# Performance work log

Measured on AMD Instinct MI355X. Metric: run time of the kernel, lower is better.

Reference implementation:

```python
import jax, jax.numpy as jnp
import numpy as np

N_NODES = 100000
N_EDGES = 1600000
IN_DIM = 128
OUT_DIM = 64
SLOPE = 0.2


def setup_inputs() -> dict:
    key = jax.random.key(0)
    k1, k2, k3, k4 = jax.random.split(key, 4)
    h = jax.random.normal(k1, (N_NODES, IN_DIM), dtype=jnp.float32)
    W = jax.random.normal(k2, (OUT_DIM, IN_DIM), dtype=jnp.float32) * (1.0 / np.sqrt(IN_DIM))
    src = jax.random.randint(k3, (N_EDGES,), 0, N_NODES, dtype=jnp.int64)
    dst = jax.random.randint(k4, (N_EDGES,), 0, N_NODES, dtype=jnp.int64)
    return {"h": h, "W": W, "src": src, "dst": dst}


def reference(h, W, src, dst):
    n = h.shape[0]
    z = h @ W.T                                   # [N, out_dim]
    z_src = z[src]                                # [E, out_dim]
    z_dst = z[dst]                                # [E, out_dim]
    e = jax.nn.leaky_relu(jnp.sum(z_src * z_dst, axis=1), negative_slope=SLOPE)  # [E]
    # segment softmax over incoming edges of each destination node
    m = jax.ops.segment_max(e, dst, num_segments=n)        # [N], -inf for isolated nodes
    ex = jnp.exp(e - m[dst])                                # [E]
    denom = jax.ops.segment_sum(ex, dst, num_segments=n)    # [N]
    alpha = ex / denom[dst]                                 # [E]
    agg = jax.ops.segment_sum(alpha[:, None] * z_src, dst, num_segments=n)  # [N, out_dim]
    return jax.nn.elu(agg)
```

## Files before the change

### kernel.cpp

```cpp
#include <hip/hip_runtime.h>
#include <hip/hip_fp16.h>
#include <math.h>

#define SLOPE 0.2f
#define LOG2E 1.4426950408889634f

typedef _Float16 half8_t __attribute__((ext_vector_type(8)));
typedef float    f32x4_t __attribute__((ext_vector_type(4)));

__device__ __forceinline__ unsigned short pk_f16(float x) {
    return __half_as_ushort(__float2half(x));
}
__device__ __forceinline__ float f16f(unsigned int bits_lo16) {
    return __half2float(__ushort_as_half((unsigned short)(bits_lo16 & 0xFFFFu)));
}

__global__ __launch_bounds__(256) void wcvt_kernel(const float* __restrict__ W,
                                                   unsigned short* __restrict__ Wh,
                                                   int total4) {
    int i = blockIdx.x * 256 + threadIdx.x;
    if (i < total4) {
        float4 w = *(const float4*)(W + (size_t)i * 4);
        ushort4 o;
        o.x = pk_f16(w.x); o.y = pk_f16(w.y);
        o.z = pk_f16(w.z); o.w = pk_f16(w.w);
        *(ushort4*)(Wh + (size_t)i * 4) = o;
    }
}

__global__ __launch_bounds__(256, 8) void gemm_hist_kernel(const float* __restrict__ h,
                                                           const unsigned short* __restrict__ Wh,
                                                           unsigned short* __restrict__ zh,
                                                           const int* __restrict__ dst,
                                                           int* __restrict__ cnt8,
                                                           unsigned short* __restrict__ rank,
                                                           int n, int ne, int nGemm) {
    int r5 = blockIdx.x % 5;
    int g5 = blockIdx.x / 5;
    if (r5 == 4) {
        int* __restrict__ cnt = cnt8 + (size_t)(g5 & 7) * n;
        int i = g5 * 256 + threadIdx.x;
        int base = i * 4;
        if (base + 3 < ne) {
            int4 d = *(const int4*)(dst + base);
            unsigned int r0 = atomicAdd(&cnt[d.x], 1);
            unsigned int r1 = atomicAdd(&cnt[d.y], 1);
            unsigned int r2 = atomicAdd(&cnt[d.z], 1);
            unsigned int r3 = atomicAdd(&cnt[d.w], 1);
            uint2 packed;
            packed.x = (r1 << 16) | (r0 & 0xFFFF);
            packed.y = (r3 << 16) | (r2 & 0xFFFF);
            *(uint2*)(rank + base) = packed;
        } else if (base < ne) {
            for (int rr = base; rr < ne; rr++)
                rank[rr] = (unsigned short)atomicAdd(&cnt[dst[rr]], 1);
        }
        return;
    }

    int gemmIdx = g5 * 4 + r5;
    int n0 = gemmIdx * 16;
    if (n0 >= n) return;
    int lane = threadIdx.x & 63;
    int wave = threadIdx.x >> 6;
    int row = lane & 15;
    int grp = lane >> 4;
    int ch0 = wave * 16;

    const float* __restrict__ hp = h + (size_t)(n0 + row) * 128 + grp * 8;
    const unsigned short* __restrict__ wp = Wh + (size_t)(ch0 + row) * 128 + grp * 8;

    f32x4_t acc = {0.f, 0.f, 0.f, 0.f};
#pragma unroll
    for (int c = 0; c < 4; c++) {
        int kc = c * 32;
        float4 a0 = *(const float4*)(hp + kc);
        float4 a1 = *(const float4*)(hp + kc + 4);
        half8_t av;
        av[0] = (_Float16)a0.x; av[1] = (_Float16)a0.y;
        av[2] = (_Float16)a0.z; av[3] = (_Float16)a0.w;
        av[4] = (_Float16)a1.x; av[5] = (_Float16)a1.y;
        av[6] = (_Float16)a1.z; av[7] = (_Float16)a1.w;
        half8_t bv = *(const half8_t*)(wp + kc);
        acc = __builtin_amdgcn_mfma_f32_16x16x32_f16(av, bv, acc, 0, 0, 0);
    }
#pragma unroll
    for (int r = 0; r < 4; r++)
        zh[(size_t)(n0 + grp * 4 + r) * 64 + ch0 + row] = pk_f16(acc[r]);
}

__global__ __launch_bounds__(256) void scan1(const int* __restrict__ cnt8,
                                             int* __restrict__ starts,
                                             int* __restrict__ bsums, int n) {
    __shared__ int ls[256];
    int tbase = blockIdx.x * 4096 + threadIdx.x * 16;
    int tot[16];
#pragma unroll
    for (int k = 0; k < 16; k++) tot[k] = 0;
    if (tbase + 15 < n) {
#pragma unroll
        for (int c = 0; c < 8; c++) {
            const int* cp = cnt8 + (size_t)c * n + tbase;
#pragma unroll
            for (int q = 0; q < 4; q++) {
                int4 v = *(const int4*)(cp + q * 4);
                tot[q * 4 + 0] += v.x; tot[q * 4 + 1] += v.y;
                tot[q * 4 + 2] += v.z; tot[q * 4 + 3] += v.w;
            }
        }
    } else {
        for (int k = 0; k < 16; k++) {
            int idx = tbase + k;
            if (idx < n)
                for (int c = 0; c < 8; c++) tot[k] += cnt8[(size_t)c * n + idx];
        }
    }
    int s = 0;
#pragma unroll
    for (int k = 0; k < 16; k++) s += tot[k];
    ls[threadIdx.x] = s;
    __syncthreads();
    for (int off = 1; off < 256; off <<= 1) {
        int t = threadIdx.x >= off ? ls[threadIdx.x - off] : 0;
        __syncthreads();
        ls[threadIdx.x] += t;
        __syncthreads();
    }
    int run = ls[threadIdx.x] - s;
    if (threadIdx.x == 255) bsums[blockIdx.x] = ls[255];
#pragma unroll
    for (int k = 0; k < 16; k++) {
        int idx = tbase + k;
        if (idx < n) starts[idx] = run;
        run += tot[k];
    }
}

__global__ __launch_bounds__(256) void scan3(int* __restrict__ starts,
                                             const int* __restrict__ bsums,
                                             int* __restrict__ cnt8,
                                             int n, int ne) {
    __shared__ int base_s;
    int i = blockIdx.x * 256 + threadIdx.x;
    if (threadIdx.x == 0) {
        int reg = (int)(blockIdx.x >> 4);
        int s = 0;
        for (int b = 0; b < reg; b++) s += bsums[b];
        base_s = s;
        if (blockIdx.x == 0) starts[n] = ne;
    }
    __syncthreads();
    if (i >= n) return;
    int b = starts[i] + base_s;
    starts[i] = b;
#pragma unroll
    for (int c = 0; c < 8; c++) {
        size_t off = (size_t)c * n + i;
        int t = cnt8[off];
        cnt8[off] = b;
        b += t;
    }
}

__global__ __launch_bounds__(256) void scatter8_kernel(const int* __restrict__ src,
                                                       const int* __restrict__ dst,
                                                       const int* __restrict__ cnt8,
                                                       const unsigned short* __restrict__ rank,
                                                       int* __restrict__ csr_src,
                                                       int n, int ne) {
    int i = blockIdx.x * 256 + threadIdx.x;
    int base = i * 8;
    if (base + 7 < ne) {
        const int* __restrict__ cb = cnt8 + (size_t)((base >> 10) & 7) * n;
        int4 s0 = *(const int4*)(src + base),  s1 = *(const int4*)(src + base + 4);
        int4 d0 = *(const int4*)(dst + base),  d1 = *(const int4*)(dst + base + 4);
        uint4 rp = *(const uint4*)(rank + base);
        csr_src[cb[d0.x] + (rp.x & 0xFFFF)] = s0.x;
        csr_src[cb[d0.y] + (rp.x >> 16)]    = s0.y;
        csr_src[cb[d0.z] + (rp.y & 0xFFFF)] = s0.z;
        csr_src[cb[d0.w] + (rp.y >> 16)]    = s0.w;
        csr_src[cb[d1.x] + (rp.z & 0xFFFF)] = s1.x;
        csr_src[cb[d1.y] + (rp.z >> 16)]    = s1.y;
        csr_src[cb[d1.z] + (rp.w & 0xFFFF)] = s1.z;
        csr_src[cb[d1.w] + (rp.w >> 16)]    = s1.w;
    } else {
        for (int e = base; e < ne; e++) {
            const int* cb = cnt8 + (size_t)((e >> 10) & 7) * n;
            csr_src[cb[dst[e]] + rank[e]] = src[e];
        }
    }
}

__global__ __launch_bounds__(256) void fused_node(const uint4* __restrict__ zh4,
                                                  const int* __restrict__ starts,
                                                  const int* __restrict__ csr_src,
                                                  float4* __restrict__ out4, int n) {
    int node = blockIdx.x * 4 + (threadIdx.x >> 6);
    if (node >= n) return;
    int lane = threadIdx.x & 63;
    int g = lane >> 3;
    int q = lane & 7;
    int rs = starts[node], re = starts[node + 1];

    uint4 zw = zh4[(size_t)node * 8 + q];
    float zdf[8];
    zdf[0] = f16f(zw.x); zdf[1] = f16f(zw.x >> 16);
    zdf[2] = f16f(zw.y); zdf[3] = f16f(zw.y >> 16);
    zdf[4] = f16f(zw.z); zdf[5] = f16f(zw.z >> 16);
    zdf[6] = f16f(zw.w); zdf[7] = f16f(zw.w >> 16);

    float m2 = -1e30f, denom = 0.f;
    float acc[8] = {};

    for (int c = rs; c < re; c += 64) {
        int j = c + lane;
        int sv = j < re ? csr_src[j] : 0;
        int cn = min(64, re - c);
        bool val0 = g < cn;
        int  s0 = __shfl(sv, val0 ? g : 0);
        uint4 w0 = zh4[(size_t)s0 * 8 + q];
        bool val1 = 8 + g < cn;
        int  s1 = __shfl(sv, val1 ? 8 + g : 0);
        uint4 w1 = zh4[(size_t)s1 * 8 + q];
        for (int k = 0; k < cn; k += 8) {
            int idx2 = k + 16 + g;
            bool val2 = idx2 < cn;
            int  s2 = __shfl(sv, val2 ? idx2 : 0);
            uint4 w2 = zh4[(size_t)s2 * 8 + q];

            float vf[8];
            vf[0] = f16f(w0.x); vf[1] = f16f(w0.x >> 16);
            vf[2] = f16f(w0.y); vf[3] = f16f(w0.y >> 16);
            vf[4] = f16f(w0.z); vf[5] = f16f(w0.z >> 16);
            vf[6] = f16f(w0.w); vf[7] = f16f(w0.w >> 16);

            float p = vf[0] * zdf[0];
#pragma unroll
            for (int jj = 1; jj < 8; jj++) p = fmaf(vf[jj], zdf[jj], p);
#pragma unroll
            for (int msk = 1; msk < 8; msk <<= 1) p += __shfl_xor(p, msk);

            float e = p > 0.f ? p : SLOPE * p;
            float e2 = e * LOG2E;
            e2 = val0 ? e2 : -2e30f;
            if (__any(e2 > m2)) {
                float mnew = fmaxf(m2, e2);
                float sc = exp2f(m2 - mnew);
                float ex = exp2f(e2 - mnew);
                denom = fmaf(denom, sc, ex);
#pragma unroll
                for (int jj = 0; jj < 8; jj++)
                    acc[jj] = fmaf(acc[jj], sc, ex * vf[jj]);
                m2 = mnew;
            } else {
                float ex = exp2f(e2 - m2);
                denom += ex;
#pragma unroll
                for (int jj = 0; jj < 8; jj++)
                    acc[jj] = fmaf(ex, vf[jj], acc[jj]);
            }
            w0 = w1; val0 = val1;
            w1 = w2; val1 = val2;
        }
    }
#pragma unroll
    for (int msk = 8; msk < 64; msk <<= 1) {
        float mo  = __shfl_xor(m2, msk);
        float dno = __shfl_xor(denom, msk);
        float ao[8];
#pragma unroll
        for (int jj = 0; jj < 8; jj++) ao[jj] = __shfl_xor(acc[jj], msk);
        float mnew = fmaxf(m2, mo);
        float ss = exp2f(m2 - mnew), so = exp2f(mo - mnew);
        denom = fmaf(denom, ss, dno * so);
#pragma unroll
        for (int jj = 0; jj < 8; jj++)
            acc[jj] = fmaf(acc[jj], ss, ao[jj] * so);
        m2 = mnew;
    }
    if (g == 0) {
        float inv = denom > 0.f ? 1.f / denom : 0.f;
        float r[8];
#pragma unroll
        for (int jj = 0; jj < 8; jj++) {
            float x = acc[jj] * inv;
            r[jj] = x > 0.f ? x : __expf(x) - 1.f;
        }
        out4[(size_t)node * 16 + q * 2 + 0] = make_float4(r[0], r[1], r[2], r[3]);
        out4[(size_t)node * 16 + q * 2 + 1] = make_float4(r[4], r[5], r[6], r[7]);
    }
}

extern "C" void kernel_launch(void* const* d_in, const int* in_sizes, int n_in,
                              void* d_out, int out_size, void* d_ws, size_t ws_size,
                              hipStream_t stream) {
    const float* h   = (const float*)d_in[0];
    const float* W   = (const float*)d_in[1];
    const int*   src = (const int*)d_in[2];
    const int*   dst = (const int*)d_in[3];
    int n  = in_sizes[0] / 128;
    int ne = in_sizes[2];

    unsigned short* zh      = (unsigned short*)d_ws;
    unsigned short* rank    = zh + (size_t)n * 64;
    int*            cnt8    = (int*)(rank + ne);
    int*            csr_src = cnt8 + (size_t)8 * n;
    unsigned short* Wh      = (unsigned short*)(csr_src + ne);
    int*            starts  = (int*)(Wh + 64 * 128);
    int*            bsums   = starts + ((n + 5) & ~3);

    int nGemm = (n + 15) / 16;
    int nbHist = (ne / 4 + 255) / 256;
    int nbTotal = nbHist * 5;
    int nb_scan = (n + 4095) / 4096;

    hipMemsetAsync(cnt8, 0, (size_t)8 * n * sizeof(int), stream);
    wcvt_kernel<<<(64 * 128 / 4 + 255) / 256, 256, 0, stream>>>(W, Wh, 64 * 128 / 4);
    gemm_hist_kernel<<<nbTotal, 256, 0, stream>>>(h, Wh, zh, dst, cnt8, rank,
                                                  n, ne, nGemm);
    scan1<<<nb_scan, 256, 0, stream>>>(cnt8, starts, bsums, n);
    scan3<<<(n + 255) / 256, 256, 0, stream>>>(starts, bsums, cnt8, n, ne);
    scatter8_kernel<<<(ne / 8 + 255) / 256, 256, 0, stream>>>(src, dst, cnt8,
                                                              rank, csr_src, n, ne);
    fused_node<<<(n + 3) / 4, 256, 0, stream>>>((const uint4*)zh, starts, csr_src,
                                                (float4*)d_out, n);
}
```

Measured before the change: 189.0 us.

## Compute edge scores with MFMA and restructure per-node softmax aggregation

```diff
diff --git a/kernel.cpp b/kernel.cpp
--- a/kernel.cpp
+++ b/kernel.cpp
@@ -6,13 +6,14 @@
 #define LOG2E 1.4426950408889634f
 
 typedef _Float16 half8_t __attribute__((ext_vector_type(8)));
+typedef _Float16 half2_t __attribute__((ext_vector_type(2)));
 typedef float    f32x4_t __attribute__((ext_vector_type(4)));
 
 __device__ __forceinline__ unsigned short pk_f16(float x) {
     return __half_as_ushort(__float2half(x));
 }
-__device__ __forceinline__ float f16f(unsigned int bits_lo16) {
-    return __half2float(__ushort_as_half((unsigned short)(bits_lo16 & 0xFFFFu)));
+__device__ __forceinline__ half2_t u2h2(unsigned int u) {
+    union { unsigned int u; half2_t h; } c; c.u = u; return c.h;
 }
 
 __global__ __launch_bounds__(256) void wcvt_kernel(const float* __restrict__ W,
@@ -191,103 +192,91 @@
     }
 }
 
-__global__ __launch_bounds__(256) void fused_node(const uint4* __restrict__ zh4,
+__global__ __launch_bounds__(256) void fused_node(const unsigned short* __restrict__ zh,
                                                   const int* __restrict__ starts,
                                                   const int* __restrict__ csr_src,
                                                   float4* __restrict__ out4, int n) {
     int node = blockIdx.x * 4 + (threadIdx.x >> 6);
     if (node >= n) return;
     int lane = threadIdx.x & 63;
-    int g = lane >> 3;
-    int q = lane & 7;
+    int g4 = lane >> 4;
+    int q4 = lane & 15;
     int rs = starts[node], re = starts[node + 1];
 
-    uint4 zw = zh4[(size_t)node * 8 + q];
-    float zdf[8];
-    zdf[0] = f16f(zw.x); zdf[1] = f16f(zw.x >> 16);
-    zdf[2] = f16f(zw.y); zdf[3] = f16f(zw.y >> 16);
-    zdf[4] = f16f(zw.z); zdf[5] = f16f(zw.z >> 16);
-    zdf[6] = f16f(zw.w); zdf[7] = f16f(zw.w >> 16);
-
-    float m2 = -1e30f, denom = 0.f;
-    float acc[8] = {};
+    const unsigned short* __restrict__ zdp = zh + (size_t)node * 64 + g4 * 8;
+    half8_t bv0 = *(const half8_t*)(zdp);
+    half8_t bv1 = *(const half8_t*)(zdp + 32);
+
+    float m = -1e30f, denom = 0.f;
+    float4 out = make_float4(0.f, 0.f, 0.f, 0.f);
 
     for (int c = rs; c < re; c += 64) {
         int j = c + lane;
         int sv = j < re ? csr_src[j] : 0;
         int cn = min(64, re - c);
-        bool val0 = g < cn;
-        int  s0 = __shfl(sv, val0 ? g : 0);
-        uint4 w0 = zh4[(size_t)s0 * 8 + q];
-        bool val1 = 8 + g < cn;
-        int  s1 = __shfl(sv, val1 ? 8 + g : 0);
-        uint4 w1 = zh4[(size_t)s1 * 8 + q];
-        for (int k = 0; k < cn; k += 8) {
-            int idx2 = k + 16 + g;
-            bool val2 = idx2 < cn;
-            int  s2 = __shfl(sv, val2 ? idx2 : 0);
-            uint4 w2 = zh4[(size_t)s2 * 8 + q];
-
-            float vf[8];
-            vf[0] = f16f(w0.x); vf[1] = f16f(w0.x >> 16);
-            vf[2] = f16f(w0.y); vf[3] = f16f(w0.y >> 16);
-            vf[4] = f16f(w0.z); vf[5] = f16f(w0.z >> 16);
-            vf[6] = f16f(w0.w); vf[7] = f16f(w0.w >> 16);
-
-            float p = vf[0] * zdf[0];
-#pragma unroll
-            for (int jj = 1; jj < 8; jj++) p = fmaf(vf[jj], zdf[jj], p);
-#pragma unroll
-            for (int msk = 1; msk < 8; msk <<= 1) p += __shfl_xor(p, msk);
-
-            float e = p > 0.f ? p : SLOPE * p;
-            float e2 = e * LOG2E;
-            e2 = val0 ? e2 : -2e30f;
-            if (__any(e2 > m2)) {
-                float mnew = fmaxf(m2, e2);
-                float sc = exp2f(m2 - mnew);
-                float ex = exp2f(e2 - mnew);
-                denom = fmaf(denom, sc, ex);
-#pragma unroll
-                for (int jj = 0; jj < 8; jj++)
-                    acc[jj] = fmaf(acc[jj], sc, ex * vf[jj]);
-                m2 = mnew;
-            } else {
-                float ex = exp2f(e2 - m2);
-                denom += ex;
-#pragma unroll
-                for (int jj = 0; jj < 8; jj++)
-                    acc[jj] = fmaf(ex, vf[jj], acc[jj]);
-            }
-            w0 = w1; val0 = val1;
-            w1 = w2; val1 = val2;
-        }
-    }
-#pragma unroll
-    for (int msk = 8; msk < 64; msk <<= 1) {
-        float mo  = __shfl_xor(m2, msk);
-        float dno = __shfl_xor(denom, msk);
-        float ao[8];
-#pragma unroll
-        for (int jj = 0; jj < 8; jj++) ao[jj] = __shfl_xor(acc[jj], msk);
-        float mnew = fmaxf(m2, mo);
-        float ss = exp2f(m2 - mnew), so = exp2f(mo - mnew);
-        denom = fmaf(denom, ss, dno * so);
-#pragma unroll
-        for (int jj = 0; jj < 8; jj++)
-            acc[jj] = fmaf(acc[jj], ss, ao[jj] * so);
-        m2 = mnew;
-    }
-    if (g == 0) {
+        for (int t = 0; t * 16 < cn; t++) {
+            int eidx = t * 16 + q4;
+            int se = __shfl(sv, eidx < cn ? eidx : 0);
+            const unsigned short* ap = zh + (size_t)se * 64 + g4 * 8;
+            half8_t a0 = *(const half8_t*)(ap);
+            half8_t a1 = *(const half8_t*)(ap + 32);
+            f32x4_t acc = {0.f, 0.f, 0.f, 0.f};
+            acc = __builtin_amdgcn_mfma_f32_16x16x32_f16(a0, bv0, acc, 0, 0, 0);
+            acc = __builtin_amdgcn_mfma_f32_16x16x32_f16(a1, bv1, acc, 0, 0, 0);
+            float e2[4];
+            float cmax = -2e30f;
+#pragma unroll
+            for (int jj = 0; jj < 4; jj++) {
+                float p = acc[jj];
+                float e = fmaxf(p, SLOPE * p) * LOG2E;
+                bool v = (t * 16 + g4 * 4 + jj) < cn;
+                e2[jj] = v ? e : -2e30f;
+                cmax = fmaxf(cmax, e2[jj]);
+            }
+            cmax = fmaxf(cmax, __shfl_xor(cmax, 16));
+            cmax = fmaxf(cmax, __shfl_xor(cmax, 32));
+            if (cmax > m) {
+                float sc = exp2f(m - cmax);
+                denom *= sc;
+                out.x *= sc; out.y *= sc; out.z *= sc; out.w *= sc;
+                m = cmax;
+            }
+            float ex[4];
+#pragma unroll
+            for (int jj = 0; jj < 4; jj++) {
+                ex[jj] = exp2f(e2[jj] - m);
+                denom += ex[jj];
+            }
+#pragma unroll
+            for (int jj = 0; jj < 4; jj++) {
+                int ei = t * 16 + g4 * 4 + jj;
+                int sa = __shfl(sv, ei < cn ? ei : 0);
+                uint2 w = *(const uint2*)(zh + (size_t)sa * 64 + q4 * 4);
+                half2_t lo = u2h2(w.x), hi = u2h2(w.y);
+                out.x = fmaf(ex[jj], (float)lo[0], out.x);
+                out.y = fmaf(ex[jj], (float)lo[1], out.y);
+                out.z = fmaf(ex[jj], (float)hi[0], out.z);
+                out.w = fmaf(ex[jj], (float)hi[1], out.w);
+            }
+        }
+    }
+#pragma unroll
+    for (int msk = 16; msk < 64; msk <<= 1) {
+        denom += __shfl_xor(denom, msk);
+        out.x += __shfl_xor(out.x, msk);
+        out.y += __shfl_xor(out.y, msk);
+        out.z += __shfl_xor(out.z, msk);
+        out.w += __shfl_xor(out.w, msk);
+    }
+    if (g4 == 0) {
         float inv = denom > 0.f ? 1.f / denom : 0.f;
-        float r[8];
-#pragma unroll
-        for (int jj = 0; jj < 8; jj++) {
-            float x = acc[jj] * inv;
-            r[jj] = x > 0.f ? x : __expf(x) - 1.f;
-        }
-        out4[(size_t)node * 16 + q * 2 + 0] = make_float4(r[0], r[1], r[2], r[3]);
-        out4[(size_t)node * 16 + q * 2 + 1] = make_float4(r[4], r[5], r[6], r[7]);
+        float4 r;
+        float x;
+        x = out.x * inv; r.x = x > 0.f ? x : __expf(x) - 1.f;
+        x = out.y * inv; r.y = x > 0.f ? x : __expf(x) - 1.f;
+        x = out.z * inv; r.z = x > 0.f ? x : __expf(x) - 1.f;
+        x = out.w * inv; r.w = x > 0.f ? x : __expf(x) - 1.f;
+        out4[(size_t)node * 16 + q4] = r;
     }
 }
 
@@ -322,6 +311,6 @@
     scan3<<<(n + 255) / 256, 256, 0, stream>>>(starts, bsums, cnt8, n, ne);
     scatter8_kernel<<<(ne / 8 + 255) / 256, 256, 0, stream>>>(src, dst, cnt8,
                                                               rank, csr_src, n, ne);
-    fused_node<<<(n + 3) / 4, 256, 0, stream>>>((const uint4*)zh, starts, csr_src,
+    fused_node<<<(n + 3) / 4, 256, 0, stream>>>(zh, starts, csr_src,
                                                 (float4*)d_out, n);
 }
```

Result: faster. 185.0 us (-2.1%).
